# Optimization experiments

Hardware: AMD Instinct MI355X
Metric: run time of the kernel (lower is better)

## Reference

```python
import jax, jax.numpy as jnp
import numpy as np
import math

B, S, D = 2, 2048, 768
H, KS, VS = 12, 64, 64
MAX_DIST, NUM_BASES, MIN_HALF_LIFE = 1000, 16, 3.0


def _exponential_basis_features():
    # positions -max_dist..max_dist, exponential basis as in RelativePositionalBias
    positions = np.arange(-MAX_DIST, MAX_DIST + 1)
    abs_pos = np.abs(positions).astype(np.float32)
    max_range = math.log2(MAX_DIST)
    half_lives = np.power(2.0, np.linspace(MIN_HALF_LIFE, max_range, NUM_BASES)).reshape(1, -1)
    feats = np.exp(-math.log(2.0) * abs_pos[:, None] / half_lives)  # [2*max_dist+1, num_bases]
    return jnp.asarray(feats, dtype=jnp.float32)


def setup_inputs() -> dict:
    key = jax.random.key(0)
    ks = jax.random.split(key, 6)
    x = jax.random.normal(ks[0], (B, S, D), dtype=jnp.float32)
    # torch nn.Linear weight convention: [out_features, in_features], applied as x @ W.T
    Wq = jax.random.normal(ks[1], (H * KS, D), dtype=jnp.float32) * 0.02
    Wk = jax.random.normal(ks[2], (H * KS, D), dtype=jnp.float32) * 0.02
    Wv = jax.random.normal(ks[3], (H * VS, D), dtype=jnp.float32) * 0.02
    # original zero-inits w_o; use small random for a non-degenerate correctness baseline
    Wo = jax.random.normal(ks[4], (D, H * VS), dtype=jnp.float32) * 0.02
    basis_weights = jax.random.normal(ks[5], (H, NUM_BASES), dtype=jnp.float32)
    basis_features = _exponential_basis_features()  # buffer (non-learned)
    return {"x": x, "Wq": Wq, "Wk": Wk, "Wv": Wv, "Wo": Wo,
            "basis_weights": basis_weights, "basis_features": basis_features}


def _relative_bias(basis_features, basis_weights, q_len, k_len):
    rel = jnp.arange(k_len)[None, :] - jnp.arange(q_len)[:, None]
    rel = jnp.clip(rel, -MAX_DIST, MAX_DIST) + MAX_DIST  # [q, k] indices
    basis = basis_features[rel]                          # [q, k, nb]
    return jnp.einsum('qkb,hb->hqk', basis, basis_weights)


def reference(x, Wq, Wk, Wv, Wo, basis_weights, basis_features):
    b, s, _ = x.shape
    q = (x @ Wq.T).reshape(b, s, H, KS)
    k = (x @ Wk.T).reshape(b, s, H, KS)
    v = (x @ Wv.T).reshape(b, s, H, VS)
    scale = math.sqrt(KS)
    scores = jnp.einsum('bqhc,bkhc->bhqk', q, k) / scale
    scores = scores + _relative_bias(basis_features, basis_weights, s, s)[None]
    attn = jax.nn.softmax(scores, axis=-1)  # dropout is identity in eval
    out = jnp.einsum('bhqk,bkhv->bqhv', attn, v).reshape(b, s, H * VS)
    out = out @ Wo.T
    return out, attn
```

## Files before the change

kernel.cpp:

```cpp
#include <hip/hip_runtime.h>

typedef _Float16 f16;
typedef __attribute__((ext_vector_type(8))) _Float16 f16x8;
typedef __attribute__((ext_vector_type(4))) float f32x4;
typedef __attribute__((ext_vector_type(16))) float f32x16;

#define B_ 2
#define S_ 2048
#define DMODEL 768
#define H_ 12
#define HS 64
#define NB_ 16
#define QKV_LD 2304

#define ZERO16 {0.f,0.f,0.f,0.f,0.f,0.f,0.f,0.f,0.f,0.f,0.f,0.f,0.f,0.f,0.f,0.f}

__global__ __launch_bounds__(256) void cast_f16_kernel(const float* __restrict__ in,
                                                       f16* __restrict__ out,
                                                       int n4, float scale) {
    int i = blockIdx.x * 256 + threadIdx.x;
    if (i >= n4) return;
    float4 v = reinterpret_cast<const float4*>(in)[i];
    union { f16 h[4]; unsigned long long u; } o;
    o.h[0] = (f16)(v.x * scale);
    o.h[1] = (f16)(v.y * scale);
    o.h[2] = (f16)(v.z * scale);
    o.h[3] = (f16)(v.w * scale);
    reinterpret_cast<unsigned long long*>(out)[i] = o.u;
}

__global__ __launch_bounds__(256) void wcast_kernel(const float* __restrict__ Wq,
                                                    const float* __restrict__ Wk,
                                                    const float* __restrict__ Wv,
                                                    f16* __restrict__ dst) {
    int i = blockIdx.x * 256 + threadIdx.x;
    const float* src;
    float scale = 1.0f;
    int j = i;
    if (i < 147456)      { src = Wq; scale = 0.18033688011112f; }
    else if (i < 294912) { src = Wk; j = i - 147456; }
    else                 { src = Wv; j = i - 294912; }
    float4 v = reinterpret_cast<const float4*>(src)[j];
    union { f16 h[4]; unsigned long long u; } o;
    o.h[0] = (f16)(v.x * scale);
    o.h[1] = (f16)(v.y * scale);
    o.h[2] = (f16)(v.z * scale);
    o.h[3] = (f16)(v.w * scale);
    reinterpret_cast<unsigned long long*>(dst)[i] = o.u;
}

__global__ __launch_bounds__(256) void bias_table_kernel(const float* __restrict__ bw,
                                                         const float* __restrict__ bf,
                                                         float* __restrict__ tab) {
    int idx = blockIdx.x * 256 + threadIdx.x;
    if (idx >= H_ * 4095) return;
    int h = idx / 4095, d = idx % 4095;
    int rel = d - 2047;
    rel = min(1000, max(-1000, rel));
    int r = rel + 1000;
    float s = 0.f;
#pragma unroll
    for (int t = 0; t < NB_; ++t) s += bf[r * NB_ + t] * bw[h * NB_ + t];
    tab[h * 4095 + d] = s * 1.44269504088896f;
}

template <typename OutT>
__global__ __launch_bounds__(256) void gemm_nt(const f16* __restrict__ A,
                                               const f16* __restrict__ Bm,
                                               OutT* __restrict__ C,
                                               int M, int N, int K, float alpha) {
    __shared__ __align__(16) f16 As[128][40];
    __shared__ __align__(16) f16 Bs[128][40];
    const int tiles_n = N >> 7;
    int tm = blockIdx.x / tiles_n, tn = blockIdx.x % tiles_n;
    int m0 = tm << 7, n0 = tn << 7;
    int t = threadIdx.x;
    int w = t >> 6, l = t & 63;
    int wr = w >> 1, wc = w & 1;
    int fr = l & 15, fc = (l >> 4) << 3;
    f32x4 acc[4][4] = {};

    for (int k0 = 0; k0 < K; k0 += 32) {
#pragma unroll
        for (int uu = 0; uu < 2; ++uu) {
            int u = t + uu * 256;
            int row = u >> 2, c = (u & 3) << 3;
            *reinterpret_cast<f16x8*>(&As[row][c]) =
                *reinterpret_cast<const f16x8*>(&A[(size_t)(m0 + row) * K + k0 + c]);
            *reinterpret_cast<f16x8*>(&Bs[row][c]) =
                *reinterpret_cast<const f16x8*>(&Bm[(size_t)(n0 + row) * K + k0 + c]);
        }
        __syncthreads();
        f16x8 af[4], bfv[4];
#pragma unroll
        for (int m = 0; m < 4; ++m)
            af[m] = *reinterpret_cast<const f16x8*>(&As[wr * 64 + m * 16 + fr][fc]);
#pragma unroll
        for (int n = 0; n < 4; ++n)
            bfv[n] = *reinterpret_cast<const f16x8*>(&Bs[wc * 64 + n * 16 + fr][fc]);
#pragma unroll
        for (int m = 0; m < 4; ++m)
#pragma unroll
            for (int n = 0; n < 4; ++n)
                acc[m][n] = __builtin_amdgcn_mfma_f32_16x16x32_f16(af[m], bfv[n], acc[m][n], 0, 0, 0);
        __syncthreads();
    }
    int cc = l & 15, cr = (l >> 4) << 2;
#pragma unroll
    for (int m = 0; m < 4; ++m)
#pragma unroll
        for (int n = 0; n < 4; ++n)
#pragma unroll
            for (int j = 0; j < 4; ++j) {
                int rg = m0 + wr * 64 + m * 16 + cr + j;
                int cg = n0 + wc * 64 + n * 16 + cc;
                C[(size_t)rg * N + cg] = (OutT)(acc[m][n][j] * alpha);
            }
}

__global__ __launch_bounds__(256, 4) void attn_kernel(const f16* __restrict__ qp,
                                                      const f16* __restrict__ kp,
                                                      const f16* __restrict__ vp,
                                                      const float* __restrict__ biasTab,
                                                      float* __restrict__ attn_out,
                                                      f16* __restrict__ ctx_out) {
    __shared__ union {
        f16 ks1[128][72];
        struct { f16 ks[64][72]; f16 vst[64][72]; } p2;
    } ar;
    __shared__ __align__(16) f16 psh[64][72];
    __shared__ float bias_l[2112];
    __shared__ float red_l[64][2];
    __shared__ float li_s[64];

    int orig = blockIdx.x;
    int blk = (orig & 7) * 96 + (orig >> 3);
    int qt = blk & 31;
    int bh = blk >> 5;
    int h = bh % H_;
    int b = bh / H_;
    int q0 = qt << 6;

    int t = threadIdx.x;
    int w = t >> 6, l = t & 63;
    int wq = w >> 1, wk = w & 1;
    int col = l & 31;
    int hi = l >> 5;
    int hi4 = hi << 2, hi8 = hi << 3;

    const size_t rowbase = (size_t)b * S_ * QKV_LD + (size_t)h * HS;

    f16x8 qf[4];
    {
        const f16* qrow = qp + rowbase + (size_t)(q0 + wq * 32 + col) * QKV_LD + hi8;
#pragma unroll
        for (int ci = 0; ci < 4; ++ci) qf[ci] = *reinterpret_cast<const f16x8*>(qrow + ci * 16);
    }

    {
        const float* bt = biasTab + h * 4095 + (1984 - q0);
        for (int i = t; i < 2111; i += 256) bias_l[i] = bt[i];
    }

    float lsum[16];
#pragma unroll
    for (int r = 0; r < 16; ++r) lsum[r] = 0.f;

    for (int kb0 = 0; kb0 < S_; kb0 += 128) {
#pragma unroll
        for (int uu = 0; uu < 4; ++uu) {
            int u = (uu << 8) + t;
            int row = u >> 3, c = (u & 7) << 3;
            *reinterpret_cast<f16x8*>(&ar.ks1[row][c]) =
                *reinterpret_cast<const f16x8*>(kp + rowbase + (size_t)(kb0 + row) * QKV_LD + c);
        }
        __syncthreads();
#pragma unroll
        for (int half = 0; half < 2; ++half) {
            f32x16 s = ZERO16;
#pragma unroll
            for (int ci = 0; ci < 4; ++ci) {
                f16x8 kf = *reinterpret_cast<const f16x8*>(
                    &ar.ks1[half * 64 + wk * 32 + col][ci * 16 + hi8]);
                s = __builtin_amdgcn_mfma_f32_32x32x16_f16(qf[ci], kf, s, 0, 0, 0);
            }
            int kcol = kb0 + half * 64 + wk * 32 + col;
            const float* bl = bias_l + (kcol + 63 - (wq * 32 + hi4));
#pragma unroll
            for (int r = 0; r < 16; ++r) {
                const int cr = (r & 3) + 8 * (r >> 2);
                lsum[r] += __builtin_amdgcn_exp2f(s[r] + bl[-cr]);
            }
        }
        __syncthreads();
    }

#pragma unroll
    for (int off = 1; off < 32; off <<= 1) {
#pragma unroll
        for (int r = 0; r < 16; ++r) lsum[r] += __shfl_xor(lsum[r], off);
    }
    if (col == 0) {
#pragma unroll
        for (int r = 0; r < 16; ++r)
            red_l[wq * 32 + (r & 3) + 8 * (r >> 2) + hi4][wk] = lsum[r];
    }
    __syncthreads();
    if (t < 64) li_s[t] = 1.0f / (red_l[t][0] + red_l[t][1]);
    __syncthreads();
    float lreg[16];
#pragma unroll
    for (int r = 0; r < 16; ++r) lreg[r] = li_s[wq * 32 + (r & 3) + 8 * (r >> 2) + hi4];

    f32x16 oacc = ZERO16;
    float* aout = attn_out + (((size_t)b * H_ + h) * S_ + q0) * S_;

    for (int kb0 = 0; kb0 < S_; kb0 += 64) {
        {
            int row = t >> 3, c = (t & 7) << 3;
            const f16* kb = kp + rowbase + (size_t)(kb0 + row) * QKV_LD + c;
            *reinterpret_cast<f16x8*>(&ar.p2.ks[row][c]) = *reinterpret_cast<const f16x8*>(kb);
            *reinterpret_cast<f16x8*>(&ar.p2.ks[row + 32][c]) =
                *reinterpret_cast<const f16x8*>(kb + (size_t)32 * QKV_LD);
            int cv = t >> 2, v0 = (t & 3) << 4;
            const f16* src = vp + rowbase + (size_t)(kb0 + cv) * QKV_LD + v0;
            __align__(16) f16 tmp[16];
            *reinterpret_cast<f16x8*>(tmp)     = *reinterpret_cast<const f16x8*>(src);
            *reinterpret_cast<f16x8*>(tmp + 8) = *reinterpret_cast<const f16x8*>(src + 8);
#pragma unroll
            for (int i2 = 0; i2 < 16; ++i2) ar.p2.vst[v0 + i2][cv] = tmp[i2];
        }
        __syncthreads();
        f32x16 s = ZERO16;
#pragma unroll
        for (int ci = 0; ci < 4; ++ci) {
            f16x8 kf = *reinterpret_cast<const f16x8*>(&ar.p2.ks[wk * 32 + col][ci * 16 + hi8]);
            s = __builtin_amdgcn_mfma_f32_32x32x16_f16(qf[ci], kf, s, 0, 0, 0);
        }
        int kcol = kb0 + wk * 32 + col;
        const float* bl = bias_l + (kcol + 63 - (wq * 32 + hi4));
#pragma unroll
        for (int r = 0; r < 16; ++r) {
            const int cr = (r & 3) + 8 * (r >> 2);
            int row = wq * 32 + cr + hi4;
            float p = __builtin_amdgcn_exp2f(s[r] + bl[-cr]) * lreg[r];
            __builtin_nontemporal_store(p, &aout[(size_t)row * S_ + kcol]);
            psh[row][wk * 32 + col] = (f16)p;
        }
        __syncthreads();
#pragma unroll
        for (int ci = 0; ci < 4; ++ci) {
            f16x8 pa = *reinterpret_cast<const f16x8*>(&psh[wq * 32 + col][ci * 16 + hi8]);
            f16x8 vf = *reinterpret_cast<const f16x8*>(&ar.p2.vst[wk * 32 + col][ci * 16 + hi8]);
            oacc = __builtin_amdgcn_mfma_f32_32x32x16_f16(pa, vf, oacc, 0, 0, 0);
        }
        __syncthreads();
    }

    {
        f16* cbase = ctx_out + ((size_t)b * S_ + q0) * DMODEL + h * HS + wk * 32 + col;
#pragma unroll
        for (int r = 0; r < 16; ++r) {
            int row = wq * 32 + (r & 3) + 8 * (r >> 2) + hi4;
            cbase[(size_t)row * DMODEL] = (f16)oacc[r];
        }
    }
}

extern "C" void kernel_launch(void* const* d_in, const int* in_sizes, int n_in,
                              void* d_out, int out_size, void* d_ws, size_t ws_size,
                              hipStream_t stream) {
    const float* x     = (const float*)d_in[0];
    const float* Wq    = (const float*)d_in[1];
    const float* Wk    = (const float*)d_in[2];
    const float* Wv    = (const float*)d_in[3];
    const float* Wo    = (const float*)d_in[4];
    const float* bw    = (const float*)d_in[5];
    const float* bfeat = (const float*)d_in[6];

    char* ws = (char*)d_ws;
    f16*   xb      = (f16*)(ws + 0);
    f16*   qkv     = (f16*)(ws + 6291456);
    f16*   ctx     = (f16*)(ws + 25165824);
    f16*   wqkv16  = (f16*)(ws + 31457280);
    f16*   wo16    = (f16*)(ws + 34996224);
    float* biasTab = (float*)(ws + 36175872);

    float* out0 = (float*)d_out;
    float* attn = out0 + (size_t)B_ * S_ * DMODEL;

    cast_f16_kernel<<<3072, 256, 0, stream>>>(x, xb, 786432, 1.0f);
    wcast_kernel<<<1728, 256, 0, stream>>>(Wq, Wk, Wv, wqkv16);
    cast_f16_kernel<<<576, 256, 0, stream>>>(Wo, wo16, 147456, 1.0f);
    bias_table_kernel<<<192, 256, 0, stream>>>(bw, bfeat, biasTab);

    gemm_nt<f16><<<32 * 18, 256, 0, stream>>>(xb, wqkv16, qkv, 4096, QKV_LD, 768, 1.0f);

    attn_kernel<<<B_ * H_ * (S_ / 64), 256, 0, stream>>>(
        qkv + 0, qkv + 768, qkv + 1536, biasTab, attn, ctx);

    gemm_nt<float><<<32 * 6, 256, 0, stream>>>(ctx, wo16, out0, 4096, DMODEL, 768, 1.0f);
}
```

Baseline: 198.0 us.

## Use direct global-to-LDS loads with XOR swizzle, pre-transpose V, fuse prep kernels

Replaces register-staged shared-memory fills in the GEMM and attention kernels with global_load_lds direct copies, using XOR-swizzled unpadded LDS layouts to avoid bank conflicts. V is transposed once in a separate kernel, so the attention pass no longer does a per-element scatter transpose into LDS. The four cast and bias-table kernels are merged into one launch. This adds an extra kernel and a V^T buffer that reuses the xb workspace region, which is safe only because xb is dead after the QKV GEMM.

```diff
diff --git a/kernel.cpp b/kernel.cpp
--- a/kernel.cpp
+++ b/kernel.cpp
@@ -15,53 +15,88 @@
 
 #define ZERO16 {0.f,0.f,0.f,0.f,0.f,0.f,0.f,0.f,0.f,0.f,0.f,0.f,0.f,0.f,0.f,0.f}
 
-__global__ __launch_bounds__(256) void cast_f16_kernel(const float* __restrict__ in,
-                                                       f16* __restrict__ out,
-                                                       int n4, float scale) {
-    int i = blockIdx.x * 256 + threadIdx.x;
-    if (i >= n4) return;
-    float4 v = reinterpret_cast<const float4*>(in)[i];
-    union { f16 h[4]; unsigned long long u; } o;
-    o.h[0] = (f16)(v.x * scale);
-    o.h[1] = (f16)(v.y * scale);
-    o.h[2] = (f16)(v.z * scale);
-    o.h[3] = (f16)(v.w * scale);
-    reinterpret_cast<unsigned long long*>(out)[i] = o.u;
-}
-
-__global__ __launch_bounds__(256) void wcast_kernel(const float* __restrict__ Wq,
-                                                    const float* __restrict__ Wk,
-                                                    const float* __restrict__ Wv,
-                                                    f16* __restrict__ dst) {
-    int i = blockIdx.x * 256 + threadIdx.x;
-    const float* src;
-    float scale = 1.0f;
-    int j = i;
-    if (i < 147456)      { src = Wq; scale = 0.18033688011112f; }
-    else if (i < 294912) { src = Wk; j = i - 147456; }
-    else                 { src = Wv; j = i - 294912; }
-    float4 v = reinterpret_cast<const float4*>(src)[j];
-    union { f16 h[4]; unsigned long long u; } o;
-    o.h[0] = (f16)(v.x * scale);
-    o.h[1] = (f16)(v.y * scale);
-    o.h[2] = (f16)(v.z * scale);
-    o.h[3] = (f16)(v.w * scale);
-    reinterpret_cast<unsigned long long*>(dst)[i] = o.u;
-}
-
-__global__ __launch_bounds__(256) void bias_table_kernel(const float* __restrict__ bw,
-                                                         const float* __restrict__ bf,
-                                                         float* __restrict__ tab) {
-    int idx = blockIdx.x * 256 + threadIdx.x;
-    if (idx >= H_ * 4095) return;
-    int h = idx / 4095, d = idx % 4095;
-    int rel = d - 2047;
-    rel = min(1000, max(-1000, rel));
-    int r = rel + 1000;
-    float s = 0.f;
-#pragma unroll
-    for (int t = 0; t < NB_; ++t) s += bf[r * NB_ + t] * bw[h * NB_ + t];
-    tab[h * 4095 + d] = s * 1.44269504088896f;
+__device__ __forceinline__ void gload16(const f16* g, f16* lds) {
+    __builtin_amdgcn_global_load_lds((const __attribute__((address_space(1))) void*)g,
+                                     (__attribute__((address_space(3))) void*)lds, 16, 0, 0);
+}
+
+__global__ __launch_bounds__(256) void prep_kernel(const float* __restrict__ x,
+                                                   const float* __restrict__ Wq,
+                                                   const float* __restrict__ Wk,
+                                                   const float* __restrict__ Wv,
+                                                   const float* __restrict__ Wo,
+                                                   const float* __restrict__ bw,
+                                                   const float* __restrict__ bf,
+                                                   f16* __restrict__ xb,
+                                                   f16* __restrict__ wqkv16,
+                                                   f16* __restrict__ wo16,
+                                                   float* __restrict__ biasTab) {
+    int bid = blockIdx.x;
+    int t = threadIdx.x;
+    if (bid < 5376) {
+        const float* src;
+        f16* dst;
+        float scale = 1.0f;
+        int i;
+        if (bid < 3072) {
+            i = bid * 256 + t; src = x; dst = xb;
+        } else if (bid < 4800) {
+            i = (bid - 3072) * 256 + t;
+            dst = wqkv16;
+            if (i < 147456)      { src = Wq; scale = 0.18033688011112f; }
+            else if (i < 294912) { src = Wk - 147456 * 4; }
+            else                 { src = Wv - 294912 * 4; }
+        } else {
+            i = (bid - 4800) * 256 + t; src = Wo; dst = wo16;
+        }
+        float4 v = reinterpret_cast<const float4*>(src)[i];
+        union { f16 h[4]; unsigned long long u; } o;
+        o.h[0] = (f16)(v.x * scale);
+        o.h[1] = (f16)(v.y * scale);
+        o.h[2] = (f16)(v.z * scale);
+        o.h[3] = (f16)(v.w * scale);
+        reinterpret_cast<unsigned long long*>(dst)[i] = o.u;
+    } else {
+        int idx = (bid - 5376) * 256 + t;
+        if (idx >= H_ * 4095) return;
+        int h = idx / 4095, d = idx % 4095;
+        int rel = min(1000, max(-1000, d - 2047));
+        int r = rel + 1000;
+        float s = 0.f;
+#pragma unroll
+        for (int tt = 0; tt < NB_; ++tt) s += bf[r * NB_ + tt] * bw[h * NB_ + tt];
+        biasTab[h * 4095 + d] = s * 1.44269504088896f;
+    }
+}
+
+__global__ __launch_bounds__(256) void vtrans_kernel(const f16* __restrict__ qkv,
+                                                     f16* __restrict__ vt) {
+    __shared__ f16 tile[64][72];
+    int blk = blockIdx.x;
+    int tb = blk & 31;
+    int bh = blk >> 5;
+    int b = bh / H_;
+    int tok0 = tb << 6;
+    int t = threadIdx.x;
+    const f16* src = qkv + (size_t)b * S_ * QKV_LD + 1536 + (bh - b * H_) * 64;
+#pragma unroll
+    for (int j = 0; j < 2; ++j) {
+        int u = t + (j << 8);
+        int r = u >> 3, c = (u & 7) << 3;
+        *reinterpret_cast<f16x8*>(&tile[r][c]) =
+            *reinterpret_cast<const f16x8*>(src + (size_t)(tok0 + r) * QKV_LD + c);
+    }
+    __syncthreads();
+    f16* dst = vt + (size_t)bh * 64 * S_ + tok0;
+#pragma unroll
+    for (int j = 0; j < 2; ++j) {
+        int u = t + (j << 8);
+        int v = u >> 3, tc = (u & 7) << 3;
+        union { f16 h8[8]; f16x8 v8; } o;
+#pragma unroll
+        for (int i = 0; i < 8; ++i) o.h8[i] = tile[tc + i][v];
+        *reinterpret_cast<f16x8*>(&dst[(size_t)v * S_ + tc]) = o.v8;
+    }
 }
 
 template <typename OutT>
@@ -69,35 +104,38 @@
                                                const f16* __restrict__ Bm,
                                                OutT* __restrict__ C,
                                                int M, int N, int K, float alpha) {
-    __shared__ __align__(16) f16 As[128][40];
-    __shared__ __align__(16) f16 Bs[128][40];
+    __shared__ __align__(16) f16 As[128 * 32];
+    __shared__ __align__(16) f16 Bs[128 * 32];
     const int tiles_n = N >> 7;
     int tm = blockIdx.x / tiles_n, tn = blockIdx.x % tiles_n;
     int m0 = tm << 7, n0 = tn << 7;
     int t = threadIdx.x;
     int w = t >> 6, l = t & 63;
     int wr = w >> 1, wc = w & 1;
-    int fr = l & 15, fc = (l >> 4) << 3;
+    int fr = l & 15, hi = l >> 4;
     f32x4 acc[4][4] = {};
 
     for (int k0 = 0; k0 < K; k0 += 32) {
 #pragma unroll
-        for (int uu = 0; uu < 2; ++uu) {
-            int u = t + uu * 256;
-            int row = u >> 2, c = (u & 3) << 3;
-            *reinterpret_cast<f16x8*>(&As[row][c]) =
-                *reinterpret_cast<const f16x8*>(&A[(size_t)(m0 + row) * K + k0 + c]);
-            *reinterpret_cast<f16x8*>(&Bs[row][c]) =
-                *reinterpret_cast<const f16x8*>(&Bm[(size_t)(n0 + row) * K + k0 + c]);
+        for (int j = 0; j < 2; ++j) {
+            int u = t + (j << 8);
+            int row = u >> 2, ch = u & 3;
+            int gcol = k0 + ((ch ^ (row & 3)) << 3);
+            gload16(&A[(size_t)(m0 + row) * K + gcol], As + (w << 9) + (j << 11));
+            gload16(&Bm[(size_t)(n0 + row) * K + gcol], Bs + (w << 9) + (j << 11));
         }
         __syncthreads();
         f16x8 af[4], bfv[4];
 #pragma unroll
-        for (int m = 0; m < 4; ++m)
-            af[m] = *reinterpret_cast<const f16x8*>(&As[wr * 64 + m * 16 + fr][fc]);
-#pragma unroll
-        for (int n = 0; n < 4; ++n)
-            bfv[n] = *reinterpret_cast<const f16x8*>(&Bs[wc * 64 + n * 16 + fr][fc]);
+        for (int m = 0; m < 4; ++m) {
+            int row = wr * 64 + m * 16 + fr;
+            af[m] = *reinterpret_cast<const f16x8*>(&As[row * 32 + ((hi ^ (fr & 3)) << 3)]);
+        }
+#pragma unroll
+        for (int n = 0; n < 4; ++n) {
+            int row = wc * 64 + n * 16 + fr;
+            bfv[n] = *reinterpret_cast<const f16x8*>(&Bs[row * 32 + ((hi ^ (fr & 3)) << 3)]);
+        }
 #pragma unroll
         for (int m = 0; m < 4; ++m)
 #pragma unroll
@@ -120,13 +158,13 @@
 
 __global__ __launch_bounds__(256, 4) void attn_kernel(const f16* __restrict__ qp,
                                                       const f16* __restrict__ kp,
-                                                      const f16* __restrict__ vp,
+                                                      const f16* __restrict__ vt,
                                                       const float* __restrict__ biasTab,
                                                       float* __restrict__ attn_out,
                                                       f16* __restrict__ ctx_out) {
-    __shared__ union {
-        f16 ks1[128][72];
-        struct { f16 ks[64][72]; f16 vst[64][72]; } p2;
+    __shared__ __align__(16) union {
+        f16 ks1[128 * 64];
+        struct { f16 ks[64 * 64]; f16 vs[64 * 64]; } p2;
     } ar;
     __shared__ __align__(16) f16 psh[64][72];
     __shared__ float bias_l[2112];
@@ -149,6 +187,7 @@
     int hi4 = hi << 2, hi8 = hi << 3;
 
     const size_t rowbase = (size_t)b * S_ * QKV_LD + (size_t)h * HS;
+    const f16* vbase = vt + (size_t)bh * HS * S_;
 
     f16x8 qf[4];
     {
@@ -168,23 +207,24 @@
 
     for (int kb0 = 0; kb0 < S_; kb0 += 128) {
 #pragma unroll
-        for (int uu = 0; uu < 4; ++uu) {
-            int u = (uu << 8) + t;
-            int row = u >> 3, c = (u & 7) << 3;
-            *reinterpret_cast<f16x8*>(&ar.ks1[row][c]) =
-                *reinterpret_cast<const f16x8*>(kp + rowbase + (size_t)(kb0 + row) * QKV_LD + c);
+        for (int j = 0; j < 4; ++j) {
+            int u = t + (j << 8);
+            int row = u >> 3, ch = u & 7;
+            gload16(kp + rowbase + (size_t)(kb0 + row) * QKV_LD + ((ch ^ (row & 7)) << 3),
+                    ar.ks1 + (w << 9) + (j << 11));
         }
         __syncthreads();
 #pragma unroll
         for (int half = 0; half < 2; ++half) {
+            int krow = half * 64 + wk * 32 + col;
             f32x16 s = ZERO16;
 #pragma unroll
             for (int ci = 0; ci < 4; ++ci) {
                 f16x8 kf = *reinterpret_cast<const f16x8*>(
-                    &ar.ks1[half * 64 + wk * 32 + col][ci * 16 + hi8]);
+                    &ar.ks1[krow * 64 + (((ci * 2 + hi) ^ (col & 7)) << 3)]);
                 s = __builtin_amdgcn_mfma_f32_32x32x16_f16(qf[ci], kf, s, 0, 0, 0);
             }
-            int kcol = kb0 + half * 64 + wk * 32 + col;
+            int kcol = kb0 + krow;
             const float* bl = bias_l + (kcol + 63 - (wq * 32 + hi4));
 #pragma unroll
             for (int r = 0; r < 16; ++r) {
@@ -216,28 +256,26 @@
     float* aout = attn_out + (((size_t)b * H_ + h) * S_ + q0) * S_;
 
     for (int kb0 = 0; kb0 < S_; kb0 += 64) {
-        {
-            int row = t >> 3, c = (t & 7) << 3;
-            const f16* kb = kp + rowbase + (size_t)(kb0 + row) * QKV_LD + c;
-            *reinterpret_cast<f16x8*>(&ar.p2.ks[row][c]) = *reinterpret_cast<const f16x8*>(kb);
-            *reinterpret_cast<f16x8*>(&ar.p2.ks[row + 32][c]) =
-                *reinterpret_cast<const f16x8*>(kb + (size_t)32 * QKV_LD);
-            int cv = t >> 2, v0 = (t & 3) << 4;
-            const f16* src = vp + rowbase + (size_t)(kb0 + cv) * QKV_LD + v0;
-            __align__(16) f16 tmp[16];
-            *reinterpret_cast<f16x8*>(tmp)     = *reinterpret_cast<const f16x8*>(src);
-            *reinterpret_cast<f16x8*>(tmp + 8) = *reinterpret_cast<const f16x8*>(src + 8);
-#pragma unroll
-            for (int i2 = 0; i2 < 16; ++i2) ar.p2.vst[v0 + i2][cv] = tmp[i2];
-        }
-        __syncthreads();
+#pragma unroll
+        for (int j = 0; j < 2; ++j) {
+            int u = t + (j << 8);
+            int row = u >> 3, ch = u & 7;
+            int sw = ((ch ^ (row & 7)) << 3);
+            gload16(kp + rowbase + (size_t)(kb0 + row) * QKV_LD + sw,
+                    ar.p2.ks + (w << 9) + (j << 11));
+            gload16(vbase + (size_t)row * S_ + kb0 + sw,
+                    ar.p2.vs + (w << 9) + (j << 11));
+        }
+        __syncthreads();
+        int krow = wk * 32 + col;
         f32x16 s = ZERO16;
 #pragma unroll
         for (int ci = 0; ci < 4; ++ci) {
-            f16x8 kf = *reinterpret_cast<const f16x8*>(&ar.p2.ks[wk * 32 + col][ci * 16 + hi8]);
+            f16x8 kf = *reinterpret_cast<const f16x8*>(
+                &ar.p2.ks[krow * 64 + (((ci * 2 + hi) ^ (col & 7)) << 3)]);
             s = __builtin_amdgcn_mfma_f32_32x32x16_f16(qf[ci], kf, s, 0, 0, 0);
         }
-        int kcol = kb0 + wk * 32 + col;
+        int kcol = kb0 + krow;
         const float* bl = bias_l + (kcol + 63 - (wq * 32 + hi4));
 #pragma unroll
         for (int r = 0; r < 16; ++r) {
@@ -251,7 +289,8 @@
 #pragma unroll
         for (int ci = 0; ci < 4; ++ci) {
             f16x8 pa = *reinterpret_cast<const f16x8*>(&psh[wq * 32 + col][ci * 16 + hi8]);
-            f16x8 vf = *reinterpret_cast<const f16x8*>(&ar.p2.vst[wk * 32 + col][ci * 16 + hi8]);
+            f16x8 vf = *reinterpret_cast<const f16x8*>(
+                &ar.p2.vs[krow * 64 + (((ci * 2 + hi) ^ (col & 7)) << 3)]);
             oacc = __builtin_amdgcn_mfma_f32_32x32x16_f16(pa, vf, oacc, 0, 0, 0);
         }
         __syncthreads();
@@ -280,6 +319,7 @@
 
     char* ws = (char*)d_ws;
     f16*   xb      = (f16*)(ws + 0);
+    f16*   vt      = (f16*)(ws + 0);
     f16*   qkv     = (f16*)(ws + 6291456);
     f16*   ctx     = (f16*)(ws + 25165824);
     f16*   wqkv16  = (f16*)(ws + 31457280);
@@ -289,15 +329,15 @@
     float* out0 = (float*)d_out;
     float* attn = out0 + (size_t)B_ * S_ * DMODEL;
 
-    cast_f16_kernel<<<3072, 256, 0, stream>>>(x, xb, 786432, 1.0f);
-    wcast_kernel<<<1728, 256, 0, stream>>>(Wq, Wk, Wv, wqkv16);
-    cast_f16_kernel<<<576, 256, 0, stream>>>(Wo, wo16, 147456, 1.0f);
-    bias_table_kernel<<<192, 256, 0, stream>>>(bw, bfeat, biasTab);
+    prep_kernel<<<5568, 256, 0, stream>>>(x, Wq, Wk, Wv, Wo, bw, bfeat,
+                                          xb, wqkv16, wo16, biasTab);
 
     gemm_nt<f16><<<32 * 18, 256, 0, stream>>>(xb, wqkv16, qkv, 4096, QKV_LD, 768, 1.0f);
 
+    vtrans_kernel<<<768, 256, 0, stream>>>(qkv, vt);
+
     attn_kernel<<<B_ * H_ * (S_ / 64), 256, 0, stream>>>(
-        qkv + 0, qkv + 768, qkv + 1536, biasTab, attn, ctx);
+        qkv + 0, qkv + 768, vt, biasTab, attn, ctx);
 
     gemm_nt<float><<<32 * 6, 256, 0, stream>>>(ctx, wo16, out0, 4096, DMODEL, 768, 1.0f);
 }
```

After: 177.7 us. 1.11x faster.
